# Kernel optimization log

Measured on AMD Instinct MI355X. Metric: run time of the kernel, lower is better.

Reference implementation:

```python
import jax, jax.numpy as jnp
import numpy as np

V, D, L, H, T, B = 128, 256, 2, 4, 4096, 8
DK, DV = 128, 256           # key_dim=0.5*D, value_dim=1.0*D (fla GLA defaults)
HK, HV = DK // H, DV // H   # 32, 64
GLN = 16.0                  # gate_logit_normalizer
CH = 64                     # chunk size
EPS = 1e-5

def layernorm(x, w, b):
    mu = x.mean(-1, keepdims=True)
    var = ((x - mu) ** 2).mean(-1, keepdims=True)
    return (x - mu) * jax.lax.rsqrt(var + EPS) * w + b

def gla_chunk(q, k, v, gk, scale):
    # q,k,gk: [B,T,H,HK], v: [B,T,H,HV]; gk are per-key log decay gates (<=0)
    B_, T_, H_, dk = q.shape
    dv = v.shape[-1]
    N = T_ // CH
    def rs(x):
        d = x.shape[-1]
        return x.reshape(B_, N, CH, H_, d).transpose(0, 3, 1, 2, 4)  # [B,H,N,C,d]
    q, k, v, gk = rs(q), rs(k), rs(v), rs(gk)
    b = jnp.cumsum(gk, axis=3)                       # inclusive within-chunk cumlog decay
    q_s = q * jnp.exp(b) * scale
    k_i = k * jnp.exp(-b)                            # for intra-chunk attention
    k_e = k * jnp.exp(b[..., -1:, :] - b)            # decayed to chunk end, for state update
    mask = jnp.tril(jnp.ones((CH, CH), bool))
    att = jnp.einsum('bhncd,bhnmd->bhncm', q_s, k_i)
    att = jnp.where(mask, att, 0.0)
    o_intra = jnp.einsum('bhncm,bhnmd->bhncd', att, v)
    g_last = jnp.exp(b[..., -1, :])                  # [B,H,N,dk] full-chunk decay
    kv = jnp.einsum('bhncd,bhnce->bhnde', k_e, v)    # [B,H,N,dk,dv]
    def step(S, inp):
        qc, gl, kvc = inp
        o = jnp.einsum('bhcd,bhde->bhce', qc, S)
        return S * gl[..., None] + kvc, o
    S0 = jnp.zeros((B_, H_, dk, dv), q.dtype)
    xs = (jnp.moveaxis(q_s, 2, 0), jnp.moveaxis(g_last, 2, 0), jnp.moveaxis(kv, 2, 0))
    _, o_inter = jax.lax.scan(step, S0, xs)
    o = o_intra + jnp.moveaxis(o_inter, 0, 2)        # [B,H,N,C,dv]
    return o.transpose(0, 2, 3, 1, 4).reshape(B_, T_, H_, dv)

def gla_attn(x, wq, wk, wv, wg, gk_w1, gk_w2, gk_b2, gnorm_w, wo):
    B_, T_, _ = x.shape
    q = (x @ wq).reshape(B_, T_, H, HK)
    k = (x @ wk).reshape(B_, T_, H, HK)
    v = (x @ wv).reshape(B_, T_, H, HV)
    gk = jax.nn.log_sigmoid(x @ gk_w1 @ gk_w2 + gk_b2) / GLN
    gk = gk.reshape(B_, T_, H, HK)
    o = gla_chunk(q, k, v, gk, HK ** -0.5)           # [B,T,H,HV]
    g = (x @ wg).reshape(B_, T_, H, HV)
    rms = jax.lax.rsqrt((o * o).mean(-1, keepdims=True) + EPS)
    o = o * rms * gnorm_w * (g * jax.nn.sigmoid(g))  # FusedRMSNormSwishGate
    return o.reshape(B_, T_, DV) @ wo

def setup_inputs() -> dict:
    key = jax.random.key(0)
    ks = jax.random.split(key, 16)
    s = 0.02
    return {
        'tokens': jax.random.randint(ks[0], (B, T), 0, V),
        'embed': jax.random.normal(ks[1], (V, D)) * s,
        'ln_w': jnp.ones((L, D)), 'ln_b': jnp.zeros((L, D)),
        'wq': jax.random.normal(ks[2], (L, D, DK)) * s,
        'wk': jax.random.normal(ks[3], (L, D, DK)) * s,
        'wv': jax.random.normal(ks[4], (L, D, DV)) * s,
        'wg': jax.random.normal(ks[5], (L, D, DV)) * s,
        'gk_w1': jax.random.normal(ks[6], (L, D, 16)) * s,
        'gk_w2': jax.random.normal(ks[7], (L, 16, DK)) * s,
        'gk_b2': jnp.zeros((L, DK)),
        'gnorm_w': jnp.ones((L, HV)),
        'wo': jax.random.normal(ks[8], (L, DV, D)) * s,
        'mlp_w1': jax.random.normal(ks[9], (L, D, 2 * D)) * s,
        'mlp_b1': jnp.zeros((L, 2 * D)),
        'mlp_w2': jax.random.normal(ks[10], (L, 2 * D, D)) * s,
        'mlp_b2': jnp.zeros((L, D)),
        'head_w': jax.random.normal(ks[11], (D, V)) * s,
        'head_b': jnp.zeros((V,)),
    }

def reference(tokens, embed, ln_w, ln_b, wq, wk, wv, wg, gk_w1, gk_w2, gk_b2,
              gnorm_w, wo, mlp_w1, mlp_b1, mlp_w2, mlp_b2, head_w, head_b):
    x = embed[tokens]
    for i in range(L):
        h = layernorm(x, ln_w[i], ln_b[i])
        x = x + gla_attn(h, wq[i], wk[i], wv[i], wg[i], gk_w1[i], gk_w2[i],
                         gk_b2[i], gnorm_w[i], wo[i])
        h = layernorm(x, ln_w[i], ln_b[i])
        x = x + jax.nn.gelu(h @ mlp_w1[i] + mlp_b1[i], approximate=False) @ mlp_w2[i] + mlp_b2[i]
    return x @ head_w + head_b
```

## Files before the change

kernel.cpp:

```cpp
#include <hip/hip_runtime.h>
#include <hip/hip_bf16.h>
#include <math.h>

namespace {

constexpr int Bq = 8, Tq = 4096, Dq = 256, Lq = 2, Hq = 4;
constexpr int DKq = 128, DVq = 256, HKq = 32, HVq = 64;
constexpr int Nq = Tq / 64;
constexpr int Mq = Bq * Tq;
constexpr int SQ = 896;
constexpr float SCALEq = 0.17677669529663688f;
constexpr int WL = 1114112;

typedef __hip_bfloat16 bf16;
typedef __attribute__((ext_vector_type(8))) short bf16x8;
typedef __attribute__((ext_vector_type(4))) float f32x4;

__device__ __forceinline__ float b2f(bf16 x) { return __bfloat162float(x); }

__device__ __forceinline__ bf16x8 ld8(const bf16* p) { return *(const bf16x8*)p; }
__device__ __forceinline__ bf16x8 ld8(const float* p) {
  const float4* q4 = (const float4*)p;
  float4 a = q4[0], b = q4[1];
  float v[8] = {a.x, a.y, a.z, a.w, b.x, b.y, b.z, b.w};
  bf16x8 r;
#pragma unroll
  for (int i = 0; i < 8; i++) r[i] = __builtin_bit_cast(short, __float2bfloat16(v[i]));
  return r;
}

__device__ __forceinline__ int swzk(int k, int row) {
  return (k & ~63) | ((((k >> 3) & 7) ^ (row & 7)) << 3) | (k & 7);
}

__device__ __forceinline__ void wsplit2(float v, bf16* hi, bf16* lo) {
  bf16 h = __float2bfloat16(v);
  *hi = h; *lo = __float2bfloat16(v - b2f(h));
}

__global__ void k_wprep(const float* __restrict__ wq, const float* __restrict__ wk,
                        const float* __restrict__ wv, const float* __restrict__ wg,
                        const float* __restrict__ g1, const float* __restrict__ g2,
                        const float* __restrict__ wo, const float* __restrict__ m1,
                        const float* __restrict__ m2, const float* __restrict__ hw,
                        bf16* __restrict__ Wt) {
  int g = blockIdx.x * 256 + threadIdx.x;
  if (g >= 2 * 540672 + 32768) return;
  if (g < 2 * 540672) {
    int l = g / 540672, r = g % 540672;
    bf16* dst = Wt + (size_t)l * WL;
    if (r < 196608) {
      int k, nf; float v;
      if (r < 32768)       { int r2 = r;          k = r2 >> 7; nf = (r2 & 127);       v = wq[l*32768 + r2]; }
      else if (r < 65536)  { int r2 = r - 32768;  k = r2 >> 7; nf = 128 + (r2 & 127); v = wk[l*32768 + r2]; }
      else if (r < 131072) { int r2 = r - 65536;  k = r2 >> 8; nf = 256 + (r2 & 255); v = wv[l*65536 + r2]; }
      else                 { int r2 = r - 131072; k = r2 >> 8; nf = 512 + (r2 & 255); v = wg[l*65536 + r2]; }
      int ks = swzk(k, nf);
      wsplit2(v, &dst[(size_t)nf*256 + ks], &dst[229376 + (size_t)nf*256 + ks]);
    } else if (r < 212992) {
      int r2 = r - 196608; int k = r2 >> 7, n = r2 & 127;
      float v = 0.f;
#pragma unroll
      for (int i = 0; i < 16; i++) v += g1[l*4096 + k*16 + i] * g2[l*2048 + i*128 + n];
      int nf = 768 + n;
      int ks = swzk(k, nf);
      wsplit2(v, &dst[(size_t)nf*256 + ks], &dst[229376 + (size_t)nf*256 + ks]);
    } else if (r < 278528) {
      int r2 = r - 212992; int k = r2 >> 8, n = r2 & 255;
      int ks = swzk(k, n);
      wsplit2(wo[l*65536 + r2], &dst[458752 + (size_t)n*256 + ks], &dst[524288 + (size_t)n*256 + ks]);
    } else if (r < 409600) {
      int r2 = r - 278528; int k = r2 >> 9, n = r2 & 511;
      int ks = swzk(k, n);
      wsplit2(m1[l*131072 + r2], &dst[589824 + (size_t)n*256 + ks], &dst[720896 + (size_t)n*256 + ks]);
    } else {
      int r2 = r - 409600; int k = r2 >> 8, n = r2 & 255;
      int ks = swzk(k, n);
      wsplit2(m2[l*131072 + r2], &dst[851968 + (size_t)n*512 + ks], &dst[983040 + (size_t)n*512 + ks]);
    }
  } else {
    int r2 = g - 2 * 540672; int k = r2 >> 7, n = r2 & 127;
    int ks = swzk(k, n);
    wsplit2(hw[r2], &Wt[2228224 + (size_t)n*256 + ks], &Wt[2228224 + 32768 + (size_t)n*256 + ks]);
  }
}

__global__ void k_embed(const int* __restrict__ tok, const float* __restrict__ emb,
                        float* __restrict__ x) {
  int row = blockIdx.x, i = threadIdx.x;
  x[(size_t)row * Dq + i] = emb[(size_t)tok[row] * Dq + i];
}

__global__ void k_ln(const float* __restrict__ x, const float* __restrict__ w,
                     const float* __restrict__ bb, bf16* __restrict__ h) {
  int row = blockIdx.x, i = threadIdx.x;
  float v = x[(size_t)row * Dq + i];
  float s = v, s2 = v * v;
#pragma unroll
  for (int o = 32; o > 0; o >>= 1) { s += __shfl_down(s, o, 64); s2 += __shfl_down(s2, o, 64); }
  __shared__ float rs[4], rs2[4];
  if ((i & 63) == 0) { rs[i >> 6] = s; rs2[i >> 6] = s2; }
  __syncthreads();
  float sum = rs[0] + rs[1] + rs[2] + rs[3];
  float sum2 = rs2[0] + rs2[1] + rs2[2] + rs2[3];
  float mu = sum * (1.f / Dq);
  float var = fmaxf(sum2 * (1.f / Dq) - mu * mu, 0.f);
  float r = rsqrtf(var + 1e-5f);
  h[(size_t)row * Dq + i] = __float2bfloat16((v - mu) * r * w[i] + bb[i]);
}

template <typename AT, typename OT, int EPI, bool BIAS, bool ACC>
__global__ __launch_bounds__(256, 3) void k_mgemm4(const AT* __restrict__ A, int lda,
                                                   const bf16* __restrict__ Wh,
                                                   const bf16* __restrict__ Wl, int ldw,
                                                   const float* __restrict__ bias,
                                                   OT* __restrict__ C, int ldc, int K) {
  __shared__ __attribute__((aligned(16))) bf16 At[128 * 64];
  __shared__ __attribute__((aligned(16))) bf16 Bh[128 * 64];
  __shared__ __attribute__((aligned(16))) bf16 Bl[128 * 64];
  int tid = threadIdx.x;
  int lane = tid & 63, wave = tid >> 6;
  int lr = lane & 15, lg = lane >> 4;
  int wm = (wave >> 1) * 64, wn = (wave & 1) * 64;
  int row0 = blockIdx.x * 128, col0 = blockIdx.y * 128;
  f32x4 acc[4][4];
#pragma unroll
  for (int m = 0; m < 4; m++)
#pragma unroll
    for (int n = 0; n < 4; n++) acc[m][n] = (f32x4){0.f, 0.f, 0.f, 0.f};

  for (int k0 = 0; k0 < K; k0 += 64) {
#pragma unroll
    for (int p = 0; p < 4; p++) {
      int cix = p * 256 + tid, r = cix >> 3, j = (cix & 7) * 8;
      bf16x8 v = ld8(A + (size_t)(row0 + r) * lda + k0 + j);
      *(bf16x8*)&At[r * 64 + swzk(j, r)] = v;
    }
#pragma unroll
    for (int p = 0; p < 4; p++) {
      int cix = p * 256 + tid, r = cix >> 3, j = (cix & 7) * 8;
      size_t go = (size_t)(col0 + r) * ldw + k0 + j;
      *(bf16x8*)&Bh[r * 64 + j] = *(const bf16x8*)(Wh + go);
      *(bf16x8*)&Bl[r * 64 + j] = *(const bf16x8*)(Wl + go);
    }
    __syncthreads();
#pragma unroll
    for (int kk = 0; kk < 64; kk += 32) {
      bf16x8 af[4], bh4[4], bl4[4];
#pragma unroll
      for (int m = 0; m < 4; m++) {
        int ar = wm + m * 16 + lr;
        af[m] = *(bf16x8*)&At[ar * 64 + swzk(kk + lg * 8, ar)];
      }
#pragma unroll
      for (int n = 0; n < 4; n++) {
        int br = wn + n * 16 + lr;
        bh4[n] = *(bf16x8*)&Bh[br * 64 + swzk(kk + lg * 8, br)];
        bl4[n] = *(bf16x8*)&Bl[br * 64 + swzk(kk + lg * 8, br)];
      }
#pragma unroll
      for (int m = 0; m < 4; m++)
#pragma unroll
        for (int n = 0; n < 4; n++) {
          acc[m][n] = __builtin_amdgcn_mfma_f32_16x16x32_bf16(af[m], bh4[n], acc[m][n], 0, 0, 0);
          acc[m][n] = __builtin_amdgcn_mfma_f32_16x16x32_bf16(af[m], bl4[n], acc[m][n], 0, 0, 0);
        }
    }
    __syncthreads();
  }
#pragma unroll
  for (int m = 0; m < 4; m++) {
#pragma unroll
    for (int n = 0; n < 4; n++) {
      int col = col0 + wn + n * 16 + lr;
      int rowb = row0 + wm + m * 16 + lg * 4;
      float bv = BIAS ? bias[col] : 0.f;
#pragma unroll
      for (int j = 0; j < 4; j++) {
        float v = acc[m][n][j] + bv;
        if (EPI == 2) v = 0.5f * v * (1.f + erff(v * 0.70710678118654752f));
        if (EPI == 3 && col >= 768) {
          float t = v + bias[col - 768];
          v = (fminf(t, 0.f) - log1pf(expf(-fabsf(t)))) * (1.f / 16.f);
        }
        size_t oi = (size_t)(rowb + j) * ldc + col;
        if constexpr (ACC) C[oi] += v;
        else if constexpr (sizeof(OT) == 2) C[oi] = __float2bfloat16(v);
        else C[oi] = v;
      }
    }
  }
}

__global__ __launch_bounds__(256) void k_intra(bf16* QKVG,
                                               bf16* __restrict__ O,
                                               bf16* __restrict__ KVt,
                                               float* __restrict__ GL) {
  int blk = blockIdx.x;
  int n = blk & 63, h = (blk >> 6) & 3, b = blk >> 8;
  __shared__ __attribute__((aligned(16))) char smem[47488];
  float* bshT = (float*)smem;
  bf16*  kvS  = (bf16*)smem;
  float* glv  = (float*)(smem + 8448);
  bf16*  vT   = (bf16*)(smem + 8576);
  bf16*  kiAH = (bf16*)(smem + 17792);
  bf16*  kiAL = (bf16*)(smem + 22400);
  bf16*  qsH  = (bf16*)(smem + 27008);
  bf16*  qsL  = (bf16*)(smem + 32128);
  bf16*  kiBH = (bf16*)(smem + 37248);
  bf16*  kiBL = (bf16*)(smem + 42368);
  bf16*  aH   = (bf16*)(smem + 27008);
  bf16*  aL   = (bf16*)(smem + 36224);
  int tid = threadIdx.x;
  int lane = tid & 63, wave = tid >> 6;
  int lr = lane & 15, lg = lane >> 4;
  size_t tbase = (size_t)b * Tq + n * 64;
  int bh = b * Hq + h;

  {
    int c = tid >> 2, dc = (tid & 3) * 8;
    bf16x8 g8 = *(const bf16x8*)(QKVG + (tbase + c) * SQ + 768 + h * HKq + dc);
#pragma unroll
    for (int i = 0; i < 8; i++) bshT[(dc + i) * 66 + c] = b2f(__builtin_bit_cast(bf16, (short)g8[i]));
  }
  __syncthreads();
#pragma unroll
  for (int dd = 0; dd < 8; dd++) {
    int d = wave * 8 + dd;
    float v = bshT[d * 66 + lane];
#pragma unroll
    for (int o = 1; o < 64; o <<= 1) {
      float t = __shfl_up(v, (unsigned)o, 64);
      if (lane >= o) v += t;
    }
    bshT[d * 66 + lane] = v;
  }
  __syncthreads();
  if (tid < 32) {
    float g = expf(bshT[tid * 66 + 63]);
    glv[tid] = g;
    GL[(size_t)(bh * Nq + n) * 32 + tid] = g;
  }
  {
    int c = tid >> 2, dc = (tid & 3) * 8;
    size_t qoff = (tbase + c) * SQ + h * HKq + dc;
    bf16x8 q8 = *(const bf16x8*)(QKVG + qoff);
    bf16x8 k8 = *(const bf16x8*)(QKVG + qoff + 128);
    bf16x8 qh8, ql8, kh8, kl8;
#pragma unroll
    for (int i = 0; i < 8; i++) {
      float bv = bshT[(dc + i) * 66 + c];
      float qv = b2f(__builtin_bit_cast(bf16, (short)q8[i])) * expf(bv) * SCALEq;
      float kv = b2f(__builtin_bit_cast(bf16, (short)k8[i])) * expf(-bv);
      bf16 qh = __float2bfloat16(qv); bf16 ql = __float2bfloat16(qv - b2f(qh));
      bf16 kh = __float2bfloat16(kv); bf16 kl = __float2bfloat16(kv - b2f(kh));
      qh8[i] = __builtin_bit_cast(short, qh); ql8[i] = __builtin_bit_cast(short, ql);
      kh8[i] = __builtin_bit_cast(short, kh); kl8[i] = __builtin_bit_cast(short, kl);
      kiAH[(dc + i) * 72 + c] = kh; kiAL[(dc + i) * 72 + c] = kl;
    }
    *(bf16x8*)&qsH[c * 40 + dc] = qh8;
    *(bf16x8*)&qsL[c * 40 + dc] = ql8;
    *(bf16x8*)&kiBH[c * 40 + dc] = kh8;
    *(bf16x8*)&kiBL[c * 40 + dc] = kl8;
    *(bf16x8*)(QKVG + qoff) = qh8;
  }
#pragma unroll
  for (int p = 0; p < 2; p++) {
    int idx = p * 256 + tid;
    int c = idx & 63, ec = (idx >> 6) * 8;
    bf16x8 v8 = *(const bf16x8*)(QKVG + (tbase + c) * SQ + 256 + h * HVq + ec);
#pragma unroll
    for (int i = 0; i < 8; i++) vT[(ec + i) * 72 + c] = __builtin_bit_cast(bf16, (short)v8[i]);
  }
  __syncthreads();
  f32x4 accq[4];
#pragma unroll
  for (int t = 0; t < 4; t++) accq[t] = (f32x4){0.f, 0.f, 0.f, 0.f};
  {
    bf16x8 afh = *(bf16x8*)&qsH[(wave * 16 + lr) * 40 + lg * 8];
    bf16x8 afl = *(bf16x8*)&qsL[(wave * 16 + lr) * 40 + lg * 8];
#pragma unroll
    for (int t = 0; t < 4; t++) {
      bf16x8 bh = *(bf16x8*)&kiBH[(t * 16 + lr) * 40 + lg * 8];
      bf16x8 bl = *(bf16x8*)&kiBL[(t * 16 + lr) * 40 + lg * 8];
      accq[t] = __builtin_amdgcn_mfma_f32_16x16x32_bf16(afh, bh, accq[t], 0, 0, 0);
      accq[t] = __builtin_amdgcn_mfma_f32_16x16x32_bf16(afh, bl, accq[t], 0, 0, 0);
      accq[t] = __builtin_amdgcn_mfma_f32_16x16x32_bf16(afl, bh, accq[t], 0, 0, 0);
    }
  }
  __syncthreads();
#pragma unroll
  for (int t = 0; t < 4; t++)
#pragma unroll
    for (int j = 0; j < 4; j++) {
      int row = wave * 16 + lg * 4 + j;
      int col = t * 16 + lr;
      float v = (col <= row) ? accq[t][j] : 0.f;
      bf16 hi = __float2bfloat16(v);
      aH[row * 72 + col] = hi;
      aL[row * 72 + col] = __float2bfloat16(v - b2f(hi));
    }
  __syncthreads();
  f32x4 acco[4];
#pragma unroll
  for (int t = 0; t < 4; t++) acco[t] = (f32x4){0.f, 0.f, 0.f, 0.f};
#pragma unroll
  for (int ks = 0; ks < 2; ks++) {
    bf16x8 ah = *(bf16x8*)&aH[(wave * 16 + lr) * 72 + ks * 32 + lg * 8];
    bf16x8 al = *(bf16x8*)&aL[(wave * 16 + lr) * 72 + ks * 32 + lg * 8];
#pragma unroll
    for (int t = 0; t < 4; t++) {
      bf16x8 bfv = *(bf16x8*)&vT[(t * 16 + lr) * 72 + ks * 32 + lg * 8];
      acco[t] = __builtin_amdgcn_mfma_f32_16x16x32_bf16(ah, bfv, acco[t], 0, 0, 0);
      acco[t] = __builtin_amdgcn_mfma_f32_16x16x32_bf16(al, bfv, acco[t], 0, 0, 0);
    }
  }
#pragma unroll
  for (int t = 0; t < 4; t++)
#pragma unroll
    for (int j = 0; j < 4; j++) {
      int row = wave * 16 + lg * 4 + j, e = t * 16 + lr;
      O[(tbase + row) * DVq + h * HVq + e] = __float2bfloat16(acco[t][j]);
    }
  f32x4 acck[2];
  acck[0] = (f32x4){0.f, 0.f, 0.f, 0.f};
  acck[1] = (f32x4){0.f, 0.f, 0.f, 0.f};
#pragma unroll
  for (int ks = 0; ks < 2; ks++) {
    bf16x8 akh = *(bf16x8*)&kiAH[((wave >> 1) * 16 + lr) * 72 + ks * 32 + lg * 8];
    bf16x8 akl = *(bf16x8*)&kiAL[((wave >> 1) * 16 + lr) * 72 + ks * 32 + lg * 8];
#pragma unroll
    for (int t = 0; t < 2; t++) {
      bf16x8 bfv = *(bf16x8*)&vT[(((wave & 1) * 2 + t) * 16 + lr) * 72 + ks * 32 + lg * 8];
      acck[t] = __builtin_amdgcn_mfma_f32_16x16x32_bf16(akh, bfv, acck[t], 0, 0, 0);
      acck[t] = __builtin_amdgcn_mfma_f32_16x16x32_bf16(akl, bfv, acck[t], 0, 0, 0);
    }
  }
#pragma unroll
  for (int t = 0; t < 2; t++)
#pragma unroll
    for (int j = 0; j < 4; j++) {
      int d = (wave >> 1) * 16 + lg * 4 + j;
      int e = ((wave & 1) * 2 + t) * 16 + lr;
      kvS[d * 72 + e] = __float2bfloat16(acck[t][j] * glv[d]);
    }
  __syncthreads();
  size_t kbase = (size_t)(bh * Nq + n) * 2048;
  {
    int d = tid >> 3, cc = (tid & 7) * 8;
    *(bf16x8*)&KVt[kbase + d * 64 + cc] = *(bf16x8*)&kvS[d * 72 + cc];
  }
}

__global__ __launch_bounds__(256) void k_inter(const bf16* __restrict__ QKVG,
                                               const float* __restrict__ GL,
                                               const bf16* __restrict__ KVt,
                                               bf16* __restrict__ O) {
  int blk = blockIdx.x;
  int es = blk & 7, h = (blk >> 3) & 3, b = blk >> 5;
  int e0 = es * 8;
  __shared__ __attribute__((aligned(16))) bf16 kvl[64 * 32 * 8];
  __shared__ float gl[64 * 32];
  __shared__ float S[64 * 32 * 8];
  int tid = threadIdx.x;
  int bh = b * Hq + h;
  const float* glp = GL + (size_t)bh * Nq * 32;
#pragma unroll
  for (int p = 0; p < 8; p++) { int i = p * 256 + tid; gl[i] = glp[i]; }
  const bf16* kvp = KVt + (size_t)bh * Nq * 2048 + e0;
#pragma unroll
  for (int p = 0; p < 8; p++) {
    int c8 = p * 256 + tid;
    *(bf16x8*)&kvl[c8 * 8] = *(const bf16x8*)(kvp + (size_t)(c8 >> 5) * 2048 + (size_t)(c8 & 31) * 64);
  }
  __syncthreads();
  {
    int pe = tid & 7, pd = tid >> 3;
    float s = 0.f;
    for (int n = 0; n < 64; n++) {
      S[(n * 32 + pd) * 8 + pe] = s;
      s = s * gl[n * 32 + pd] + b2f(kvl[(n * 32 + pd) * 8 + pe]);
    }
  }
  __syncthreads();
  int c = tid >> 2, ep = tid & 3;
  for (int n = 0; n < 64; n++) {
    size_t tbase = (size_t)b * Tq + n * 64;
    const bf16* qp = QKVG + (tbase + c) * SQ + h * HKq;
    const float* Sp = &S[n * 256];
    float a0 = 0.f, a1 = 0.f;
#pragma unroll
    for (int j = 0; j < 4; j++) {
      bf16x8 q8 = *(const bf16x8*)(qp + j * 8);
#pragma unroll
      for (int i = 0; i < 8; i++) {
        float qf = b2f(__builtin_bit_cast(bf16, (short)q8[i]));
        int d = j * 8 + i;
        a0 += qf * Sp[d * 8 + ep];
        a1 += qf * Sp[d * 8 + ep + 4];
      }
    }
    size_t oi = (tbase + c) * DVq + h * HVq + e0 + ep;
    O[oi] = __float2bfloat16(b2f(O[oi]) + a0);
    O[oi + 4] = __float2bfloat16(b2f(O[oi + 4]) + a1);
  }
}

__global__ void k_gate(bf16* __restrict__ O, const bf16* __restrict__ QKVG,
                       const float* __restrict__ gnw) {
  int row = blockIdx.x, tid = threadIdx.x;
  int e = tid & 63;
  float o = b2f(O[(size_t)row * DVq + tid]);
  float s = o * o;
#pragma unroll
  for (int of = 32; of > 0; of >>= 1) s += __shfl_xor(s, of, 64);
  float r = rsqrtf(s * (1.f / 64.f) + 1e-5f);
  float g = b2f(QKVG[(size_t)row * SQ + 512 + tid]);
  float sw = g / (1.f + expf(-g));
  O[(size_t)row * DVq + tid] = __float2bfloat16(o * r * gnw[e] * sw);
}

}

extern "C" void kernel_launch(void* const* d_in, const int* in_sizes, int n_in,
                              void* d_out, int out_size, void* d_ws, size_t ws_size,
                              hipStream_t stream) {
  const int*   tok  = (const int*)d_in[0];
  const float* emb  = (const float*)d_in[1];
  const float* ln_w = (const float*)d_in[2];
  const float* ln_b = (const float*)d_in[3];
  const float* wq   = (const float*)d_in[4];
  const float* wk   = (const float*)d_in[5];
  const float* wv   = (const float*)d_in[6];
  const float* wg   = (const float*)d_in[7];
  const float* gkw1 = (const float*)d_in[8];
  const float* gkw2 = (const float*)d_in[9];
  const float* gkb2 = (const float*)d_in[10];
  const float* gnw  = (const float*)d_in[11];
  const float* wo   = (const float*)d_in[12];
  const float* mw1  = (const float*)d_in[13];
  const float* mb1  = (const float*)d_in[14];
  const float* mw2  = (const float*)d_in[15];
  const float* mb2  = (const float*)d_in[16];
  const float* hw   = (const float*)d_in[17];
  const float* hb   = (const float*)d_in[18];

  if (ws_size < 134217728u) return;
  char* w = (char*)d_ws;
  float* X    = (float*)w;
  bf16*  Ob   = (bf16*)(w + 33554432);
  bf16*  Hbf  = Ob;
  bf16*  QKVG = (bf16*)(w + 50331648);
  bf16*  KVt  = (bf16*)(w + 109051904);
  float* GLb  = (float*)(w + 117440512);
  bf16*  Wt   = (bf16*)(w + 117702656);
  bf16*  MLPH = QKVG;

  dim3 blk(256);
  k_wprep<<<4353, blk, 0, stream>>>(wq, wk, wv, wg, gkw1, gkw2, wo, mw1, mw2, hw, Wt);
  k_embed<<<Mq, blk, 0, stream>>>(tok, emb, X);

  for (int l = 0; l < Lq; l++) {
    const bf16* Wl = Wt + (size_t)l * WL;
    k_ln<<<Mq, blk, 0, stream>>>(X, ln_w + l * Dq, ln_b + l * Dq, Hbf);
    k_mgemm4<bf16, bf16, 3, false, false><<<dim3(256, 7), blk, 0, stream>>>(Hbf, 256, Wl, Wl + 229376, 256, gkb2 + l * DKq, QKVG, SQ, 256);
    k_intra<<<Bq * Hq * Nq, blk, 0, stream>>>(QKVG, Ob, KVt, GLb);
    k_inter<<<Bq * Hq * 8, blk, 0, stream>>>(QKVG, GLb, KVt, Ob);
    k_gate<<<Mq, blk, 0, stream>>>(Ob, QKVG, gnw + l * HVq);
    k_mgemm4<bf16, float, 0, false, true><<<dim3(256, 2), blk, 0, stream>>>(Ob, 256, Wl + 458752, Wl + 524288, 256, nullptr, X, 256, 256);
    k_ln<<<Mq, blk, 0, stream>>>(X, ln_w + l * Dq, ln_b + l * Dq, Hbf);
    k_mgemm4<bf16, bf16, 2, true, false><<<dim3(256, 4), blk, 0, stream>>>(Hbf, 256, Wl + 589824, Wl + 720896, 256, mb1 + l * 2 * Dq, MLPH, 512, 256);
    k_mgemm4<bf16, float, 0, true, true><<<dim3(256, 2), blk, 0, stream>>>(MLPH, 512, Wl + 851968, Wl + 983040, 512, mb2 + l * Dq, X, 256, 512);
  }
  k_mgemm4<float, float, 0, true, false><<<dim3(256, 1), blk, 0, stream>>>(X, 256, Wt + 2228224, Wt + 2228224 + 32768, 256, hb, (float*)d_out, 128, 256);
}
```

Before: 690.8 us.

## Pre-pack weights in MFMA fragment order and load B directly from global

```diff
diff --git a/kernel.cpp b/kernel.cpp
--- a/kernel.cpp
+++ b/kernel.cpp
@@ -31,6 +31,13 @@
 
 __device__ __forceinline__ int swzk(int k, int row) {
   return (k & ~63) | ((((k >> 3) & 7) ^ (row & 7)) << 3) | (k & 7);
+}
+
+__device__ __forceinline__ size_t fidx(int n, int k, int K) {
+  int ct = n >> 7, nt = (n >> 4) & 7, lr = n & 15;
+  int k0 = k >> 6, kk = (k >> 5) & 1, lg = (k >> 3) & 3, e = k & 7;
+  int fi = ((ct * (K >> 6) + k0) * 2 + kk) * 8 + nt;
+  return (size_t)fi * 512 + (lg * 16 + lr) * 8 + e;
 }
 
 __device__ __forceinline__ void wsplit2(float v, bf16* hi, bf16* lo) {
@@ -55,33 +62,32 @@
       else if (r < 65536)  { int r2 = r - 32768;  k = r2 >> 7; nf = 128 + (r2 & 127); v = wk[l*32768 + r2]; }
       else if (r < 131072) { int r2 = r - 65536;  k = r2 >> 8; nf = 256 + (r2 & 255); v = wv[l*65536 + r2]; }
       else                 { int r2 = r - 131072; k = r2 >> 8; nf = 512 + (r2 & 255); v = wg[l*65536 + r2]; }
-      int ks = swzk(k, nf);
-      wsplit2(v, &dst[(size_t)nf*256 + ks], &dst[229376 + (size_t)nf*256 + ks]);
+      size_t fo = fidx(nf, k, 256);
+      wsplit2(v, &dst[fo], &dst[229376 + fo]);
     } else if (r < 212992) {
       int r2 = r - 196608; int k = r2 >> 7, n = r2 & 127;
       float v = 0.f;
 #pragma unroll
       for (int i = 0; i < 16; i++) v += g1[l*4096 + k*16 + i] * g2[l*2048 + i*128 + n];
-      int nf = 768 + n;
-      int ks = swzk(k, nf);
-      wsplit2(v, &dst[(size_t)nf*256 + ks], &dst[229376 + (size_t)nf*256 + ks]);
+      size_t fo = fidx(768 + n, k, 256);
+      wsplit2(v, &dst[fo], &dst[229376 + fo]);
     } else if (r < 278528) {
       int r2 = r - 212992; int k = r2 >> 8, n = r2 & 255;
-      int ks = swzk(k, n);
-      wsplit2(wo[l*65536 + r2], &dst[458752 + (size_t)n*256 + ks], &dst[524288 + (size_t)n*256 + ks]);
+      size_t fo = fidx(n, k, 256);
+      wsplit2(wo[l*65536 + r2], &dst[458752 + fo], &dst[524288 + fo]);
     } else if (r < 409600) {
       int r2 = r - 278528; int k = r2 >> 9, n = r2 & 511;
-      int ks = swzk(k, n);
-      wsplit2(m1[l*131072 + r2], &dst[589824 + (size_t)n*256 + ks], &dst[720896 + (size_t)n*256 + ks]);
+      size_t fo = fidx(n, k, 256);
+      wsplit2(m1[l*131072 + r2], &dst[589824 + fo], &dst[720896 + fo]);
     } else {
       int r2 = r - 409600; int k = r2 >> 8, n = r2 & 255;
-      int ks = swzk(k, n);
-      wsplit2(m2[l*131072 + r2], &dst[851968 + (size_t)n*512 + ks], &dst[983040 + (size_t)n*512 + ks]);
+      size_t fo = fidx(n, k, 512);
+      wsplit2(m2[l*131072 + r2], &dst[851968 + fo], &dst[983040 + fo]);
     }
   } else {
     int r2 = g - 2 * 540672; int k = r2 >> 7, n = r2 & 127;
-    int ks = swzk(k, n);
-    wsplit2(hw[r2], &Wt[2228224 + (size_t)n*256 + ks], &Wt[2228224 + 32768 + (size_t)n*256 + ks]);
+    size_t fo = fidx(n, k, 256);
+    wsplit2(hw[r2], &Wt[2228224 + fo], &Wt[2228224 + 32768 + fo]);
   }
 }
 
@@ -110,19 +116,18 @@
 }
 
 template <typename AT, typename OT, int EPI, bool BIAS, bool ACC>
-__global__ __launch_bounds__(256, 3) void k_mgemm4(const AT* __restrict__ A, int lda,
-                                                   const bf16* __restrict__ Wh,
-                                                   const bf16* __restrict__ Wl, int ldw,
+__global__ __launch_bounds__(256, 4) void k_mgemm7(const AT* __restrict__ A, int lda,
+                                                   const bf16* __restrict__ Whf,
+                                                   const bf16* __restrict__ Wlf,
                                                    const float* __restrict__ bias,
                                                    OT* __restrict__ C, int ldc, int K) {
   __shared__ __attribute__((aligned(16))) bf16 At[128 * 64];
-  __shared__ __attribute__((aligned(16))) bf16 Bh[128 * 64];
-  __shared__ __attribute__((aligned(16))) bf16 Bl[128 * 64];
   int tid = threadIdx.x;
   int lane = tid & 63, wave = tid >> 6;
   int lr = lane & 15, lg = lane >> 4;
   int wm = (wave >> 1) * 64, wn = (wave & 1) * 64;
-  int row0 = blockIdx.x * 128, col0 = blockIdx.y * 128;
+  int row0 = blockIdx.x * 128;
+  int ct = blockIdx.y, nk = K >> 6;
   f32x4 acc[4][4];
 #pragma unroll
   for (int m = 0; m < 4; m++)
@@ -130,35 +135,31 @@
     for (int n = 0; n < 4; n++) acc[m][n] = (f32x4){0.f, 0.f, 0.f, 0.f};
 
   for (int k0 = 0; k0 < K; k0 += 64) {
+    int k0i = k0 >> 6;
 #pragma unroll
     for (int p = 0; p < 4; p++) {
       int cix = p * 256 + tid, r = cix >> 3, j = (cix & 7) * 8;
       bf16x8 v = ld8(A + (size_t)(row0 + r) * lda + k0 + j);
       *(bf16x8*)&At[r * 64 + swzk(j, r)] = v;
     }
-#pragma unroll
-    for (int p = 0; p < 4; p++) {
-      int cix = p * 256 + tid, r = cix >> 3, j = (cix & 7) * 8;
-      size_t go = (size_t)(col0 + r) * ldw + k0 + j;
-      *(bf16x8*)&Bh[r * 64 + j] = *(const bf16x8*)(Wh + go);
-      *(bf16x8*)&Bl[r * 64 + j] = *(const bf16x8*)(Wl + go);
-    }
     __syncthreads();
 #pragma unroll
     for (int kk = 0; kk < 64; kk += 32) {
+      int fb = ((ct * nk + k0i) * 2 + (kk >> 5)) * 8 + (wn >> 4);
+      const bf16* bhp = Whf + (size_t)fb * 512 + lane * 8;
+      const bf16* blp = Wlf + (size_t)fb * 512 + lane * 8;
       bf16x8 af[4], bh4[4], bl4[4];
+#pragma unroll
+      for (int n = 0; n < 4; n++) {
+        bh4[n] = *(const bf16x8*)(bhp + n * 512);
+        bl4[n] = *(const bf16x8*)(blp + n * 512);
+      }
 #pragma unroll
       for (int m = 0; m < 4; m++) {
         int ar = wm + m * 16 + lr;
         af[m] = *(bf16x8*)&At[ar * 64 + swzk(kk + lg * 8, ar)];
       }
 #pragma unroll
-      for (int n = 0; n < 4; n++) {
-        int br = wn + n * 16 + lr;
-        bh4[n] = *(bf16x8*)&Bh[br * 64 + swzk(kk + lg * 8, br)];
-        bl4[n] = *(bf16x8*)&Bl[br * 64 + swzk(kk + lg * 8, br)];
-      }
-#pragma unroll
       for (int m = 0; m < 4; m++)
 #pragma unroll
         for (int n = 0; n < 4; n++) {
@@ -172,7 +173,7 @@
   for (int m = 0; m < 4; m++) {
 #pragma unroll
     for (int n = 0; n < 4; n++) {
-      int col = col0 + wn + n * 16 + lr;
+      int col = ct * 128 + wn + n * 16 + lr;
       int rowb = row0 + wm + m * 16 + lg * 4;
       float bv = BIAS ? bias[col] : 0.f;
 #pragma unroll
@@ -463,14 +464,14 @@
   for (int l = 0; l < Lq; l++) {
     const bf16* Wl = Wt + (size_t)l * WL;
     k_ln<<<Mq, blk, 0, stream>>>(X, ln_w + l * Dq, ln_b + l * Dq, Hbf);
-    k_mgemm4<bf16, bf16, 3, false, false><<<dim3(256, 7), blk, 0, stream>>>(Hbf, 256, Wl, Wl + 229376, 256, gkb2 + l * DKq, QKVG, SQ, 256);
+    k_mgemm7<bf16, bf16, 3, false, false><<<dim3(256, 7), blk, 0, stream>>>(Hbf, 256, Wl, Wl + 229376, gkb2 + l * DKq, QKVG, SQ, 256);
     k_intra<<<Bq * Hq * Nq, blk, 0, stream>>>(QKVG, Ob, KVt, GLb);
     k_inter<<<Bq * Hq * 8, blk, 0, stream>>>(QKVG, GLb, KVt, Ob);
     k_gate<<<Mq, blk, 0, stream>>>(Ob, QKVG, gnw + l * HVq);
-    k_mgemm4<bf16, float, 0, false, true><<<dim3(256, 2), blk, 0, stream>>>(Ob, 256, Wl + 458752, Wl + 524288, 256, nullptr, X, 256, 256);
+    k_mgemm7<bf16, float, 0, false, true><<<dim3(256, 2), blk, 0, stream>>>(Ob, 256, Wl + 458752, Wl + 524288, nullptr, X, 256, 256);
     k_ln<<<Mq, blk, 0, stream>>>(X, ln_w + l * Dq, ln_b + l * Dq, Hbf);
-    k_mgemm4<bf16, bf16, 2, true, false><<<dim3(256, 4), blk, 0, stream>>>(Hbf, 256, Wl + 589824, Wl + 720896, 256, mb1 + l * 2 * Dq, MLPH, 512, 256);
-    k_mgemm4<bf16, float, 0, true, true><<<dim3(256, 2), blk, 0, stream>>>(MLPH, 512, Wl + 851968, Wl + 983040, 512, mb2 + l * Dq, X, 256, 512);
-  }
-  k_mgemm4<float, float, 0, true, false><<<dim3(256, 1), blk, 0, stream>>>(X, 256, Wt + 2228224, Wt + 2228224 + 32768, 256, hb, (float*)d_out, 128, 256);
-}
+    k_mgemm7<bf16, bf16, 2, true, false><<<dim3(256, 4), blk, 0, stream>>>(Hbf, 256, Wl + 589824, Wl + 720896, mb1 + l * 2 * Dq, MLPH, 512, 256);
+    k_mgemm7<bf16, float, 0, true, true><<<dim3(256, 2), blk, 0, stream>>>(MLPH, 512, Wl + 851968, Wl + 983040, mb2 + l * Dq, X, 256, 512);
+  }
+  k_mgemm7<float, float, 0, true, false><<<dim3(256, 1), blk, 0, stream>>>(X, 256, Wt + 2228224, Wt + 2228224 + 32768, hb, (float*)d_out, 128, 256);
+}
```

New measurement: 673.4 us. -2.5%, faster.
